# Optimization experiments

Hardware: AMD Instinct MI355X
Metric: run time of the kernel (lower is better)

Reference implementation:

```python
import jax, jax.numpy as jnp
import numpy as np

N_NODES = 50000
N_EDGES = 800000
F_IN = 64
F_OUT = 64
SELF_LOOP_W = 2.0  # GCNConv improved=True


def setup_inputs() -> dict:
    key = jax.random.key(0)
    k1, k2, k3 = jax.random.split(key, 3)
    x = jax.random.normal(k1, (N_NODES, F_IN), dtype=jnp.float32)
    edge_index = jax.random.randint(k2, (2, N_EDGES), 0, N_NODES, dtype=jnp.int64)
    W = jax.random.normal(k3, (F_IN, F_OUT), dtype=jnp.float32) / np.sqrt(F_IN)
    b = jnp.zeros((F_OUT,), dtype=jnp.float32)
    return {"x": x, "edge_index": edge_index, "W": W, "b": b}


def reference(x, edge_index, W, b):
    N = x.shape[0]
    E = edge_index.shape[1]
    src, dst = edge_index[0], edge_index[1]
    # add self loops with weight 2.0 (improved=True)
    loop = jnp.arange(N, dtype=src.dtype)
    src_f = jnp.concatenate([src, loop])
    dst_f = jnp.concatenate([dst, loop])
    w_edge = jnp.concatenate([jnp.ones((E,), x.dtype), jnp.full((N,), SELF_LOOP_W, x.dtype)])
    # symmetric normalization: deg over target nodes (PyG gcn_norm)
    deg = jax.ops.segment_sum(w_edge, dst_f, num_segments=N)
    dinv = jnp.where(deg > 0, deg ** -0.5, 0.0)
    norm = dinv[src_f] * w_edge * dinv[dst_f]  # [E+N]
    # dense transform, then gather-scale-scatter
    h = x @ W  # [N, F_OUT]
    agg = jax.ops.segment_sum(norm[:, None] * h[src_f], dst_f, num_segments=N)
    out = jax.nn.relu(agg + b)
    return jax.nn.log_softmax(out, axis=1)
```

## Files before the change

### kernel.cpp

```cpp
#include <hip/hip_runtime.h>
#include <hip/hip_fp16.h>

#define N_NODES 50000
#define N_EDGES 800000
#define F 64
#define NB ((N_NODES + 255) / 256)
#define NBUCK 98
#define BSHIFT 9
#define BCAP 12288
#define P1_BLOCKS ((N_EDGES + 1023) / 1024)
#define NPB 32


union H2U { __half2 h; unsigned u; };

__global__ __launch_bounds__(1024) void k_p1c(const int* __restrict__ src,
                                              const int* __restrict__ dst,
                                              int* __restrict__ bcur,
                                              int* __restrict__ staging,
                                              const float4* __restrict__ x4,
                                              uint2* __restrict__ xh8) {
    __shared__ int lcnt[NBUCK];
    __shared__ int lbase[NBUCK];
    int t = threadIdx.x;
    int g = blockIdx.x * 1024 + t;
    if (t < NBUCK) lcnt[t] = 0;
    if (g < N_NODES * (F / 4)) {
        float4 v = x4[g];
        H2U a, b;
        a.h = __float22half2_rn(make_float2(v.x, v.y));
        b.h = __float22half2_rn(make_float2(v.z, v.w));
        uint2 o; o.x = a.u; o.y = b.u;
        xh8[g] = o;
    }
    __syncthreads();
    int s = 0, d = 0, bk = 0, rank = 0;
    bool valid = (g < N_EDGES);
    if (valid) {
        s = src[g]; d = dst[g];
        bk = d >> BSHIFT;
        rank = atomicAdd(&lcnt[bk], 1);
    }
    __syncthreads();
    if (t < NBUCK && lcnt[t]) lbase[t] = atomicAdd(&bcur[t], lcnt[t]);
    __syncthreads();
    if (valid)
        staging[bk * BCAP + lbase[bk] + rank] = ((d & 511) << 16) | s;
}

__global__ __launch_bounds__(1024) void k_p23(const int* __restrict__ staging,
                                              const int* __restrict__ bcur,
                                              int* __restrict__ offsets,
                                              int* __restrict__ counts,
                                              float* __restrict__ dinv,
                                              int* __restrict__ pack) {
    __shared__ int ncnt[512];
    __shared__ int lcur[512];
    int t = threadIdx.x;
    int b = blockIdx.x;
    int nb0 = b << BSHIFT;
    if (t < 512) ncnt[t] = 0;
    __syncthreads();
    int beg = b * BCAP, end = beg + bcur[b];
    for (int i = beg + t; i < end; i += 1024)
        atomicAdd(&ncnt[staging[i] >> 16], 1);
    __syncthreads();
    int c = (t < 512) ? ncnt[t] : 0;
    for (int off = 1; off < 512; off <<= 1) {
        int u = (t < 512 && t >= off) ? ncnt[t - off] : 0;
        __syncthreads();
        if (t < 512) ncnt[t] += u;
        __syncthreads();
    }
    if (t < 512) {
        int goff = beg + (ncnt[t] - c);
        lcur[t] = goff;
        int node = nb0 + t;
        if (node < N_NODES) {
            offsets[node] = goff;
            counts[node]  = c;
            dinv[node]    = rsqrtf((float)c + 2.0f);
        }
    }
    __syncthreads();
    for (int i = beg + t; i < end; i += 1024) {
        int v = staging[i];
        int pos = atomicAdd(&lcur[v >> 16], 1);
        pack[pos] = v & 0xFFFF;
    }
}

__global__ __launch_bounds__(512) void k_agg(const float* __restrict__ x,
                                             const __half* __restrict__ xh,
                                             const float* __restrict__ dinv,
                                             const int* __restrict__ offsets,
                                             const int* __restrict__ counts,
                                             const int* __restrict__ pack,
                                             const float* __restrict__ W,
                                             const float* __restrict__ bias,
                                             float* __restrict__ out) {
    __shared__ unsigned sWu[F * F / 2];
    __shared__ float srow[NPB][F];
    int t = threadIdx.x;
    for (int i = t; i < F * F / 2; i += 512) {
        int p = i >> 6, c = i & 63;
        H2U u;
        u.h = __float22half2_rn(make_float2(W[(2 * p) * F + c], W[(2 * p + 1) * F + c]));
        sWu[i] = u.u;
    }
    __syncthreads();

    int wid = t >> 6, lane = t & 63;
    int qe = lane >> 4, qc = lane & 15;
    int nbase = blockIdx.x * NPB + wid * 4;
    const uint2* xh8 = reinterpret_cast<const uint2*>(xh);

    int4   off4 = *reinterpret_cast<const int4*>(offsets + nbase);
    int4   cnt4 = *reinterpret_cast<const int4*>(counts + nbase);
    float4 dv4  = *reinterpret_cast<const float4*>(dinv + nbase);
    int   begs[4] = { off4.x, off4.y, off4.z, off4.w };
    int   degs[4] = { cnt4.x, cnt4.y, cnt4.z, cnt4.w };
    float dns[4]  = { dv4.x, dv4.y, dv4.z, dv4.w };
#pragma unroll
    for (int i = 0; i < 4; ++i)
        if (nbase + i >= N_NODES) { degs[i] = 0; dns[i] = 0.f; begs[i] = 0; }

    int pls[4]; float nms[4];
#pragma unroll
    for (int i = 0; i < 4; ++i) {
        int s = 0; float nm = 0.f;
        if (lane < degs[i]) {
            s = pack[begs[i] + lane];
            nm = dns[i] * dinv[s];
        }
        pls[i] = s; nms[i] = nm;
    }

    float acc[4][4];
#pragma unroll
    for (int i = 0; i < 4; ++i)
#pragma unroll
        for (int j = 0; j < 4; ++j) acc[i][j] = 0.f;

    int lim = max(max(degs[0], degs[1]), max(degs[2], degs[3]));
    lim = min(lim, 64);
    for (int r = 0; r < lim; r += 8) {
        int e0 = r + qe, e1 = r + 4 + qe;
        uint2 v[4][2]; float m[4][2];
#pragma unroll
        for (int i = 0; i < 4; ++i) {
            int s0 = __shfl(pls[i], e0); m[i][0] = __shfl(nms[i], e0);
            int s1 = __shfl(pls[i], e1); m[i][1] = __shfl(nms[i], e1);
            v[i][0] = xh8[(size_t)s0 * 16 + qc];
            v[i][1] = xh8[(size_t)s1 * 16 + qc];
        }
#pragma unroll
        for (int i = 0; i < 4; ++i)
#pragma unroll
            for (int j = 0; j < 2; ++j) {
                H2U u0, u1;
                u0.u = v[i][j].x; u1.u = v[i][j].y;
                float2 f0 = __half22float2(u0.h);
                float2 f1 = __half22float2(u1.h);
                float mm = m[i][j];
                acc[i][0] = fmaf(mm, f0.x, acc[i][0]);
                acc[i][1] = fmaf(mm, f0.y, acc[i][1]);
                acc[i][2] = fmaf(mm, f1.x, acc[i][2]);
                acc[i][3] = fmaf(mm, f1.y, acc[i][3]);
            }
    }
#pragma unroll
    for (int i = 0; i < 4; ++i) {
        int dend = begs[i] + degs[i];
        for (int base = begs[i] + 64; base < dend; base += 8) {
            int e0 = base + qe, e1 = base + 4 + qe;
            int s0 = 0, s1 = 0; float m0 = 0.f, m1 = 0.f;
            if (e0 < dend) { s0 = pack[e0]; m0 = dns[i] * dinv[s0]; }
            if (e1 < dend) { s1 = pack[e1]; m1 = dns[i] * dinv[s1]; }
            uint2 r0 = xh8[(size_t)s0 * 16 + qc];
            uint2 r1 = xh8[(size_t)s1 * 16 + qc];
            H2U u0, u1; float2 f;
            u0.u = r0.x; u1.u = r0.y;
            f = __half22float2(u0.h); acc[i][0] = fmaf(m0, f.x, acc[i][0]); acc[i][1] = fmaf(m0, f.y, acc[i][1]);
            f = __half22float2(u1.h); acc[i][2] = fmaf(m0, f.x, acc[i][2]); acc[i][3] = fmaf(m0, f.y, acc[i][3]);
            u0.u = r1.x; u1.u = r1.y;
            f = __half22float2(u0.h); acc[i][0] = fmaf(m1, f.x, acc[i][0]); acc[i][1] = fmaf(m1, f.y, acc[i][1]);
            f = __half22float2(u1.h); acc[i][2] = fmaf(m1, f.x, acc[i][2]); acc[i][3] = fmaf(m1, f.y, acc[i][3]);
        }
    }

#pragma unroll
    for (int i = 0; i < 4; ++i)
#pragma unroll
        for (int j = 0; j < 4; ++j) {
            acc[i][j] += __shfl_xor(acc[i][j], 16);
            acc[i][j] += __shfl_xor(acc[i][j], 32);
        }

    if (qe == 0) {
#pragma unroll
        for (int i = 0; i < 4; ++i) {
            int n = nbase + i;
            if (n < N_NODES) {
                float c2 = 2.0f * dns[i] * dns[i];
                float4 xv = reinterpret_cast<const float4*>(x + (size_t)n * F)[qc];
                float4 w;
                w.x = fmaf(c2, xv.x, acc[i][0]);
                w.y = fmaf(c2, xv.y, acc[i][1]);
                w.z = fmaf(c2, xv.z, acc[i][2]);
                w.w = fmaf(c2, xv.w, acc[i][3]);
                *reinterpret_cast<float4*>(&srow[wid * 4 + i][qc * 4]) = w;
            }
        }
    }

    asm volatile("s_waitcnt lgkmcnt(0)" ::: "memory");

    float bl = bias[lane];
    float y0 = bl, y1 = bl, y2 = bl, y3 = bl;
#pragma unroll 4
    for (int j = 0; j < 16; ++j) {
        float4 r0 = *reinterpret_cast<const float4*>(&srow[wid * 4 + 0][j * 4]);
        float4 r1 = *reinterpret_cast<const float4*>(&srow[wid * 4 + 1][j * 4]);
        float4 r2 = *reinterpret_cast<const float4*>(&srow[wid * 4 + 2][j * 4]);
        float4 r3 = *reinterpret_cast<const float4*>(&srow[wid * 4 + 3][j * 4]);
        H2U ua, ub;
        ua.u = sWu[(2 * j) * F + lane];
        ub.u = sWu[(2 * j + 1) * F + lane];
        float2 wab = __half22float2(ua.h);
        float2 wcd = __half22float2(ub.h);
        y0 = fmaf(r0.x, wab.x, y0); y0 = fmaf(r0.y, wab.y, y0); y0 = fmaf(r0.z, wcd.x, y0); y0 = fmaf(r0.w, wcd.y, y0);
        y1 = fmaf(r1.x, wab.x, y1); y1 = fmaf(r1.y, wab.y, y1); y1 = fmaf(r1.z, wcd.x, y1); y1 = fmaf(r1.w, wcd.y, y1);
        y2 = fmaf(r2.x, wab.x, y2); y2 = fmaf(r2.y, wab.y, y2); y2 = fmaf(r2.z, wcd.x, y2); y2 = fmaf(r2.w, wcd.y, y2);
        y3 = fmaf(r3.x, wab.x, y3); y3 = fmaf(r3.y, wab.y, y3); y3 = fmaf(r3.z, wcd.x, y3); y3 = fmaf(r3.w, wcd.y, y3);
    }

    float ys[4] = { y0, y1, y2, y3 };
#pragma unroll
    for (int i = 0; i < 4; ++i) {
        float y = fmaxf(ys[i], 0.0f);
        float mx = y;
#pragma unroll
        for (int off = 32; off > 0; off >>= 1)
            mx = fmaxf(mx, __shfl_xor(mx, off));
        float ex = __expf(y - mx);
        float ss = ex;
#pragma unroll
        for (int off = 32; off > 0; off >>= 1)
            ss += __shfl_xor(ss, off);
        int n = nbase + i;
        if (n < N_NODES) out[n * F + lane] = y - mx - __logf(ss);
    }
}


__global__ void k_count_b(const int* __restrict__ dst, int* __restrict__ counts) {
    int e = blockIdx.x * blockDim.x + threadIdx.x;
    if (e < N_EDGES) atomicAdd(&counts[dst[e]], 1);
}
__global__ __launch_bounds__(256) void k_blocksum(const int* __restrict__ counts,
                                                  int* __restrict__ bs) {
    __shared__ int sh[256];
    int t = threadIdx.x;
    int g = blockIdx.x * 256 + t;
    int v = (g < N_NODES) ? counts[g] : 0;
    sh[t] = v;
    __syncthreads();
    for (int off = 128; off > 0; off >>= 1) {
        if (t < off) sh[t] += sh[t + off];
        __syncthreads();
    }
    if (t == 0) bs[blockIdx.x] = sh[0];
}
__global__ __launch_bounds__(256) void k_scanblocks(int* __restrict__ bs) {
    __shared__ int sh[256];
    int t = threadIdx.x;
    int v = (t < NB) ? bs[t] : 0;
    sh[t] = v;
    __syncthreads();
    for (int off = 1; off < 256; off <<= 1) {
        int u = (t >= off) ? sh[t - off] : 0;
        __syncthreads();
        sh[t] += u;
        __syncthreads();
    }
    if (t < NB) bs[t] = sh[t] - v;
}
__global__ __launch_bounds__(256) void k_offsets_b(int* __restrict__ counts,
                                                   const int* __restrict__ bs,
                                                   int* __restrict__ offsets,
                                                   float* __restrict__ dinv) {
    __shared__ int sh[256];
    int t = threadIdx.x;
    int g = blockIdx.x * 256 + t;
    int c = (g < N_NODES) ? counts[g] : 0;
    sh[t] = c;
    __syncthreads();
    for (int off = 1; off < 256; off <<= 1) {
        int u = (t >= off) ? sh[t - off] : 0;
        __syncthreads();
        sh[t] += u;
        __syncthreads();
    }
    int excl = sh[t] - c + bs[blockIdx.x];
    if (g < N_NODES) {
        offsets[g] = excl;
        counts[g]  = excl;
        dinv[g]    = rsqrtf((float)c + 2.0f);
    }
    if (g == 0) offsets[N_NODES] = N_EDGES;
}
__global__ void k_fill_b(const int* __restrict__ src, const int* __restrict__ dst,
                         int* __restrict__ cursor, int* __restrict__ sorted_src) {
    int e = blockIdx.x * blockDim.x + threadIdx.x;
    if (e < N_EDGES) {
        int pos = atomicAdd(&cursor[dst[e]], 1);
        sorted_src[pos] = src[e];
    }
}
__global__ __launch_bounds__(256) void k_agg_b(const float* __restrict__ x,
                                               const float* __restrict__ dinv,
                                               const int* __restrict__ offsets,
                                               const int* __restrict__ sorted_src,
                                               const float* __restrict__ W,
                                               const float* __restrict__ b,
                                               float* __restrict__ out) {
    __shared__ float sW[F * F];
    __shared__ float srow[4][F];
    int t = threadIdx.x;
    for (int i = t; i < F * F; i += 256) sW[i] = W[i];
    int wid = t >> 6, lane = t & 63;
    int n = blockIdx.x * 4 + wid;
    int qe = lane >> 4, qc = lane & 15;
    float dn = dinv[n];
    int beg = offsets[n], end = offsets[n + 1];
    float4 acc = make_float4(0.f, 0.f, 0.f, 0.f);
    for (int base = beg; base < end; base += 4) {
        int e = base + qe;
        int s = n; float nm = 0.f;
        if (e < end) { s = sorted_src[e]; nm = dn * dinv[s]; }
        float4 v = reinterpret_cast<const float4*>(x + (size_t)s * F)[qc];
        acc.x = fmaf(nm, v.x, acc.x); acc.y = fmaf(nm, v.y, acc.y);
        acc.z = fmaf(nm, v.z, acc.z); acc.w = fmaf(nm, v.w, acc.w);
    }
    acc.x += __shfl_xor(acc.x, 16); acc.y += __shfl_xor(acc.y, 16);
    acc.z += __shfl_xor(acc.z, 16); acc.w += __shfl_xor(acc.w, 16);
    acc.x += __shfl_xor(acc.x, 32); acc.y += __shfl_xor(acc.y, 32);
    acc.z += __shfl_xor(acc.z, 32); acc.w += __shfl_xor(acc.w, 32);
    float c2 = 2.0f * dn * dn;
    float4 xv = reinterpret_cast<const float4*>(x + (size_t)n * F)[qc];
    acc.x = fmaf(c2, xv.x, acc.x); acc.y = fmaf(c2, xv.y, acc.y);
    acc.z = fmaf(c2, xv.z, acc.z); acc.w = fmaf(c2, xv.w, acc.w);
    if (qe == 0) reinterpret_cast<float4*>(&srow[wid][0])[qc] = acc;
    __syncthreads();
    float y = b[lane];
#pragma unroll
    for (int k = 0; k < F; ++k) y = fmaf(srow[wid][k], sW[k * F + lane], y);
    y = fmaxf(y, 0.0f);
    float m = y;
#pragma unroll
    for (int off = 32; off > 0; off >>= 1) m = fmaxf(m, __shfl_xor(m, off));
    float ex = __expf(y - m);
    float ss = ex;
#pragma unroll
    for (int off = 32; off > 0; off >>= 1) ss += __shfl_xor(ss, off);
    out[n * F + lane] = y - m - __logf(ss);
}


__global__ void k_init_deg_f(float* __restrict__ deg) {
    int i = blockIdx.x * blockDim.x + threadIdx.x;
    if (i < N_NODES) deg[i] = 2.0f;
}
__global__ void k_count_f(const int* __restrict__ dst, float* __restrict__ deg) {
    int e = blockIdx.x * blockDim.x + threadIdx.x;
    if (e < N_EDGES) atomicAdd(&deg[dst[e]], 1.0f);
}
__global__ void k_dinv_f(float* __restrict__ deg) {
    int i = blockIdx.x * blockDim.x + threadIdx.x;
    if (i < N_NODES) deg[i] = rsqrtf(deg[i]);
}
__global__ void k_selfinit_f(const float* __restrict__ x, const float* __restrict__ dinv,
                             float* __restrict__ agg) {
    int t = blockIdx.x * blockDim.x + threadIdx.x;
    if (t >= N_NODES * (F / 4)) return;
    int n = t >> 4;
    float d = dinv[n];
    float c = 2.0f * d * d;
    float4 v = reinterpret_cast<const float4*>(x)[t];
    float4 o; o.x = c*v.x; o.y = c*v.y; o.z = c*v.z; o.w = c*v.w;
    reinterpret_cast<float4*>(agg)[t] = o;
}
__global__ __launch_bounds__(256) void k_scatter_f(const int* __restrict__ src,
                                                   const int* __restrict__ dst,
                                                   const float* __restrict__ x,
                                                   const float* __restrict__ dinv,
                                                   float* __restrict__ agg) {
    int wave = (blockIdx.x * blockDim.x + threadIdx.x) >> 6;
    int lane = threadIdx.x & 63;
    if (wave >= N_EDGES) return;
    int s = src[wave], d = dst[wave];
    atomicAdd(&agg[d * F + lane], dinv[s] * dinv[d] * x[s * F + lane]);
}
__global__ __launch_bounds__(256) void k_final_f(const float* __restrict__ W,
                                                 const float* __restrict__ b,
                                                 float* __restrict__ out) {
    __shared__ float sW[F * F];
    __shared__ float srow[4][F];
    int t = threadIdx.x;
    for (int i = t; i < F * F; i += 256) sW[i] = W[i];
    int wid = t >> 6, lane = t & 63;
    int n = blockIdx.x * 4 + wid;
    float rv = out[n * F + lane];
    srow[wid][lane] = rv;
    __syncthreads();
    float y = b[lane];
#pragma unroll
    for (int k = 0; k < F; ++k) y = fmaf(srow[wid][k], sW[k * F + lane], y);
    y = fmaxf(y, 0.0f);
    float m = y;
#pragma unroll
    for (int off = 32; off > 0; off >>= 1) m = fmaxf(m, __shfl_xor(m, off));
    float ex = __expf(y - m);
    float ss = ex;
#pragma unroll
    for (int off = 32; off > 0; off >>= 1) ss += __shfl_xor(ss, off);
    out[n * F + lane] = y - m - __logf(ss);
}


extern "C" void kernel_launch(void* const* d_in, const int* in_sizes, int n_in,
                              void* d_out, int out_size, void* d_ws, size_t ws_size,
                              hipStream_t stream) {
    const float* x    = (const float*)d_in[0];
    const int*   eidx = (const int*)d_in[1];
    const float* W    = (const float*)d_in[2];
    const float* b    = (const float*)d_in[3];
    const int* src = eidx;
    const int* dst = eidx + N_EDGES;
    float* out = (float*)d_out;

    const size_t NEED_A5 = 11818112;
    const size_t NEED_B  = 3801040;

    if (ws_size >= NEED_A5) {
        char* ws = (char*)d_ws;
        int*    offsets = (int*)(ws);
        int*    counts  = (int*)(ws + 200064);
        float*  dinv    = (float*)(ws + 400128);
        int*    bcur    = (int*)(ws + 600192);
        int*    pack    = (int*)(ws + 601216);
        __half* xh      = (__half*)(ws + 5418112);
        int*    staging = (int*)d_out;

        hipMemsetAsync(bcur, 0, NBUCK * sizeof(int), stream);
        k_p1c<<<P1_BLOCKS, 1024, 0, stream>>>(src, dst, bcur, staging,
                                              (const float4*)x, (uint2*)xh);
        k_p23<<<NBUCK, 1024, 0, stream>>>(staging, bcur, offsets, counts, dinv, pack);
        k_agg<<<(N_NODES + NPB - 1) / NPB, 512, 0, stream>>>(
            x, xh, dinv, offsets, counts, pack, W, b, out);
    } else if (ws_size >= NEED_B) {
        char* ws = (char*)d_ws;
        int*   counts     = (int*)(ws);
        int*   offsets    = (int*)(ws + 200000);
        float* dinv       = (float*)(ws + 400016);
        int*   bs         = (int*)(ws + 600016);
        int*   sorted_src = (int*)(ws + 601040);

        hipMemsetAsync(counts, 0, N_NODES * sizeof(int), stream);
        k_count_b<<<(N_EDGES + 255) / 256, 256, 0, stream>>>(dst, counts);
        k_blocksum<<<NB, 256, 0, stream>>>(counts, bs);
        k_scanblocks<<<1, 256, 0, stream>>>(bs);
        k_offsets_b<<<NB, 256, 0, stream>>>(counts, bs, offsets, dinv);
        k_fill_b<<<(N_EDGES + 255) / 256, 256, 0, stream>>>(src, dst, counts, sorted_src);
        k_agg_b<<<N_NODES / 4, 256, 0, stream>>>(x, dinv, offsets, sorted_src, W, b, out);
    } else {
        float* deg = (float*)d_ws;
        k_init_deg_f<<<(N_NODES + 255) / 256, 256, 0, stream>>>(deg);
        k_count_f<<<(N_EDGES + 255) / 256, 256, 0, stream>>>(dst, deg);
        k_dinv_f<<<(N_NODES + 255) / 256, 256, 0, stream>>>(deg);
        k_selfinit_f<<<(N_NODES * (F / 4) + 255) / 256, 256, 0, stream>>>(x, deg, out);
        k_scatter_f<<<(N_EDGES * 64 + 255) / 256, 256, 0, stream>>>(src, dst, x, deg, out);
        k_final_f<<<N_NODES / 4, 256, 0, stream>>>(W, b, out);
    }
}
```

Before: 89.97 us.

## Precompute half-precision edge norms in pack and simplify aggregation to lane-per-feature

The fused bucket-sort kernel is split in two. A new pass computes each edge's symmetric norm (dinv[src]*dinv[dst]) and packs it as fp16 into the upper bits of the pack entry next to the source index. Aggregation drops the shuffle-based 16-lane quad scheme and uses one lane per feature with a wave-uniform loop over edges, reading 2-byte fp16 features per lane and the self-loop term from the fp16 copy of x. The memset becomes a tiny init kernel. This removes per-edge dinv gathers in the hot loop, but adds a kernel launch and lowers precision for norms and the self term.

After: 108.6 us. +20.7%, slower.

```diff
diff --git a/kernel.cpp b/kernel.cpp
--- a/kernel.cpp
+++ b/kernel.cpp
@@ -14,6 +14,11 @@
 
 union H2U { __half2 h; unsigned u; };
 
+__global__ void k_init(int* __restrict__ bcur) {
+    int t = threadIdx.x;
+    if (t < NBUCK) bcur[t] = 0;
+}
+
 __global__ __launch_bounds__(1024) void k_p1c(const int* __restrict__ src,
                                               const int* __restrict__ dst,
                                               int* __restrict__ bcur,
@@ -48,14 +53,12 @@
         staging[bk * BCAP + lbase[bk] + rank] = ((d & 511) << 16) | s;
 }
 
-__global__ __launch_bounds__(1024) void k_p23(const int* __restrict__ staging,
-                                              const int* __restrict__ bcur,
-                                              int* __restrict__ offsets,
-                                              int* __restrict__ counts,
-                                              float* __restrict__ dinv,
-                                              int* __restrict__ pack) {
+__global__ __launch_bounds__(1024) void k_p2(const int* __restrict__ staging,
+                                             const int* __restrict__ bcur,
+                                             int* __restrict__ offsets,
+                                             int* __restrict__ counts,
+                                             float* __restrict__ dinv) {
     __shared__ int ncnt[512];
-    __shared__ int lcur[512];
     int t = threadIdx.x;
     int b = blockIdx.x;
     int nb0 = b << BSHIFT;
@@ -73,29 +76,48 @@
         __syncthreads();
     }
     if (t < 512) {
-        int goff = beg + (ncnt[t] - c);
-        lcur[t] = goff;
         int node = nb0 + t;
         if (node < N_NODES) {
-            offsets[node] = goff;
+            offsets[node] = beg + (ncnt[t] - c);
             counts[node]  = c;
             dinv[node]    = rsqrtf((float)c + 2.0f);
         }
     }
-    __syncthreads();
+}
+
+__global__ __launch_bounds__(1024) void k_p3(const int* __restrict__ staging,
+                                             const int* __restrict__ bcur,
+                                             const int* __restrict__ offsets,
+                                             const float* __restrict__ dinv,
+                                             unsigned* __restrict__ pack) {
+    __shared__ int lcur[512];
+    __shared__ float sdinv[512];
+    int t = threadIdx.x;
+    int b = blockIdx.x;
+    int nb0 = b << BSHIFT;
+    if (t < 512) {
+        int node = nb0 + t;
+        lcur[t]  = (node < N_NODES) ? offsets[node] : 0;
+        sdinv[t] = (node < N_NODES) ? dinv[node] : 0.f;
+    }
+    __syncthreads();
+    int beg = b * BCAP, end = beg + bcur[b];
     for (int i = beg + t; i < end; i += 1024) {
         int v = staging[i];
-        int pos = atomicAdd(&lcur[v >> 16], 1);
-        pack[pos] = v & 0xFFFF;
-    }
-}
-
-__global__ __launch_bounds__(512) void k_agg(const float* __restrict__ x,
-                                             const __half* __restrict__ xh,
+        int dl = v >> 16;
+        int s  = v & 0xFFFF;
+        int pos = atomicAdd(&lcur[dl], 1);
+        float nm = dinv[s] * sdinv[dl];
+        unsigned hv = __half_as_ushort(__float2half_rn(nm));
+        pack[pos] = (hv << 16) | (unsigned)s;
+    }
+}
+
+__global__ __launch_bounds__(512) void k_agg(const __half* __restrict__ xh,
                                              const float* __restrict__ dinv,
                                              const int* __restrict__ offsets,
                                              const int* __restrict__ counts,
-                                             const int* __restrict__ pack,
+                                             const unsigned* __restrict__ pack,
                                              const float* __restrict__ W,
                                              const float* __restrict__ bias,
                                              float* __restrict__ out) {
@@ -111,106 +133,44 @@
     __syncthreads();
 
     int wid = t >> 6, lane = t & 63;
-    int qe = lane >> 4, qc = lane & 15;
     int nbase = blockIdx.x * NPB + wid * 4;
-    const uint2* xh8 = reinterpret_cast<const uint2*>(xh);
-
-    int4   off4 = *reinterpret_cast<const int4*>(offsets + nbase);
-    int4   cnt4 = *reinterpret_cast<const int4*>(counts + nbase);
-    float4 dv4  = *reinterpret_cast<const float4*>(dinv + nbase);
-    int   begs[4] = { off4.x, off4.y, off4.z, off4.w };
-    int   degs[4] = { cnt4.x, cnt4.y, cnt4.z, cnt4.w };
-    float dns[4]  = { dv4.x, dv4.y, dv4.z, dv4.w };
-#pragma unroll
-    for (int i = 0; i < 4; ++i)
-        if (nbase + i >= N_NODES) { degs[i] = 0; dns[i] = 0.f; begs[i] = 0; }
-
-    int pls[4]; float nms[4];
+
 #pragma unroll
     for (int i = 0; i < 4; ++i) {
-        int s = 0; float nm = 0.f;
-        if (lane < degs[i]) {
-            s = pack[begs[i] + lane];
-            nm = dns[i] * dinv[s];
+        int n = nbase + i;
+        int beg = 0, deg = 0; float dn = 0.f;
+        if (n < N_NODES) {
+            beg = __builtin_amdgcn_readfirstlane(offsets[n]);
+            deg = __builtin_amdgcn_readfirstlane(counts[n]);
+            dn  = dinv[n];
         }
-        pls[i] = s; nms[i] = nm;
-    }
-
-    float acc[4][4];
-#pragma unroll
-    for (int i = 0; i < 4; ++i)
-#pragma unroll
-        for (int j = 0; j < 4; ++j) acc[i][j] = 0.f;
-
-    int lim = max(max(degs[0], degs[1]), max(degs[2], degs[3]));
-    lim = min(lim, 64);
-    for (int r = 0; r < lim; r += 8) {
-        int e0 = r + qe, e1 = r + 4 + qe;
-        uint2 v[4][2]; float m[4][2];
-#pragma unroll
-        for (int i = 0; i < 4; ++i) {
-            int s0 = __shfl(pls[i], e0); m[i][0] = __shfl(nms[i], e0);
-            int s1 = __shfl(pls[i], e1); m[i][1] = __shfl(nms[i], e1);
-            v[i][0] = xh8[(size_t)s0 * 16 + qc];
-            v[i][1] = xh8[(size_t)s1 * 16 + qc];
+
+        float a0 = 0.f, a1 = 0.f, a2 = 0.f, a3 = 0.f;
+        int e = 0;
+        for (; e + 4 <= deg; e += 4) {
+            unsigned p0 = pack[beg + e + 0];
+            unsigned p1 = pack[beg + e + 1];
+            unsigned p2 = pack[beg + e + 2];
+            unsigned p3 = pack[beg + e + 3];
+            float v0 = __half2float(xh[(size_t)(p0 & 0xFFFF) * F + lane]);
+            float v1 = __half2float(xh[(size_t)(p1 & 0xFFFF) * F + lane]);
+            float v2 = __half2float(xh[(size_t)(p2 & 0xFFFF) * F + lane]);
+            float v3 = __half2float(xh[(size_t)(p3 & 0xFFFF) * F + lane]);
+            a0 = fmaf(__half2float(__ushort_as_half((unsigned short)(p0 >> 16))), v0, a0);
+            a1 = fmaf(__half2float(__ushort_as_half((unsigned short)(p1 >> 16))), v1, a1);
+            a2 = fmaf(__half2float(__ushort_as_half((unsigned short)(p2 >> 16))), v2, a2);
+            a3 = fmaf(__half2float(__ushort_as_half((unsigned short)(p3 >> 16))), v3, a3);
         }
-#pragma unroll
-        for (int i = 0; i < 4; ++i)
-#pragma unroll
-            for (int j = 0; j < 2; ++j) {
-                H2U u0, u1;
-                u0.u = v[i][j].x; u1.u = v[i][j].y;
-                float2 f0 = __half22float2(u0.h);
-                float2 f1 = __half22float2(u1.h);
-                float mm = m[i][j];
-                acc[i][0] = fmaf(mm, f0.x, acc[i][0]);
-                acc[i][1] = fmaf(mm, f0.y, acc[i][1]);
-                acc[i][2] = fmaf(mm, f1.x, acc[i][2]);
-                acc[i][3] = fmaf(mm, f1.y, acc[i][3]);
-            }
-    }
-#pragma unroll
-    for (int i = 0; i < 4; ++i) {
-        int dend = begs[i] + degs[i];
-        for (int base = begs[i] + 64; base < dend; base += 8) {
-            int e0 = base + qe, e1 = base + 4 + qe;
-            int s0 = 0, s1 = 0; float m0 = 0.f, m1 = 0.f;
-            if (e0 < dend) { s0 = pack[e0]; m0 = dns[i] * dinv[s0]; }
-            if (e1 < dend) { s1 = pack[e1]; m1 = dns[i] * dinv[s1]; }
-            uint2 r0 = xh8[(size_t)s0 * 16 + qc];
-            uint2 r1 = xh8[(size_t)s1 * 16 + qc];
-            H2U u0, u1; float2 f;
-            u0.u = r0.x; u1.u = r0.y;
-            f = __half22float2(u0.h); acc[i][0] = fmaf(m0, f.x, acc[i][0]); acc[i][1] = fmaf(m0, f.y, acc[i][1]);
-            f = __half22float2(u1.h); acc[i][2] = fmaf(m0, f.x, acc[i][2]); acc[i][3] = fmaf(m0, f.y, acc[i][3]);
-            u0.u = r1.x; u1.u = r1.y;
-            f = __half22float2(u0.h); acc[i][0] = fmaf(m1, f.x, acc[i][0]); acc[i][1] = fmaf(m1, f.y, acc[i][1]);
-            f = __half22float2(u1.h); acc[i][2] = fmaf(m1, f.x, acc[i][2]); acc[i][3] = fmaf(m1, f.y, acc[i][3]);
+        for (; e < deg; ++e) {
+            unsigned p0 = pack[beg + e];
+            float v0 = __half2float(xh[(size_t)(p0 & 0xFFFF) * F + lane]);
+            a0 = fmaf(__half2float(__ushort_as_half((unsigned short)(p0 >> 16))), v0, a0);
         }
-    }
-
-#pragma unroll
-    for (int i = 0; i < 4; ++i)
-#pragma unroll
-        for (int j = 0; j < 4; ++j) {
-            acc[i][j] += __shfl_xor(acc[i][j], 16);
-            acc[i][j] += __shfl_xor(acc[i][j], 32);
-        }
-
-    if (qe == 0) {
-#pragma unroll
-        for (int i = 0; i < 4; ++i) {
-            int n = nbase + i;
-            if (n < N_NODES) {
-                float c2 = 2.0f * dns[i] * dns[i];
-                float4 xv = reinterpret_cast<const float4*>(x + (size_t)n * F)[qc];
-                float4 w;
-                w.x = fmaf(c2, xv.x, acc[i][0]);
-                w.y = fmaf(c2, xv.y, acc[i][1]);
-                w.z = fmaf(c2, xv.z, acc[i][2]);
-                w.w = fmaf(c2, xv.w, acc[i][3]);
-                *reinterpret_cast<float4*>(&srow[wid * 4 + i][qc * 4]) = w;
-            }
+        float acc = (a0 + a1) + (a2 + a3);
+        if (n < N_NODES) {
+            float sv = __half2float(xh[(size_t)n * F + lane]);
+            acc = fmaf(2.0f * dn * dn, sv, acc);
+            srow[wid * 4 + i][lane] = acc;
         }
     }
 
@@ -440,25 +400,26 @@
     const int* dst = eidx + N_EDGES;
     float* out = (float*)d_out;
 
-    const size_t NEED_A5 = 11818112;
+    const size_t NEED_A8 = 11818112;
     const size_t NEED_B  = 3801040;
 
-    if (ws_size >= NEED_A5) {
+    if (ws_size >= NEED_A8) {
         char* ws = (char*)d_ws;
-        int*    offsets = (int*)(ws);
-        int*    counts  = (int*)(ws + 200064);
-        float*  dinv    = (float*)(ws + 400128);
-        int*    bcur    = (int*)(ws + 600192);
-        int*    pack    = (int*)(ws + 601216);
-        __half* xh      = (__half*)(ws + 5418112);
-        int*    staging = (int*)d_out;
-
-        hipMemsetAsync(bcur, 0, NBUCK * sizeof(int), stream);
+        int*      offsets = (int*)(ws);
+        int*      counts  = (int*)(ws + 200064);
+        float*    dinv    = (float*)(ws + 400128);
+        int*      bcur    = (int*)(ws + 600192);
+        unsigned* pack    = (unsigned*)(ws + 601216);
+        __half*   xh      = (__half*)(ws + 5418112);
+        int*      staging = (int*)d_out;
+
+        k_init<<<1, 128, 0, stream>>>(bcur);
         k_p1c<<<P1_BLOCKS, 1024, 0, stream>>>(src, dst, bcur, staging,
                                               (const float4*)x, (uint2*)xh);
-        k_p23<<<NBUCK, 1024, 0, stream>>>(staging, bcur, offsets, counts, dinv, pack);
+        k_p2<<<NBUCK, 1024, 0, stream>>>(staging, bcur, offsets, counts, dinv);
+        k_p3<<<NBUCK, 1024, 0, stream>>>(staging, bcur, offsets, dinv, pack);
         k_agg<<<(N_NODES + NPB - 1) / NPB, 512, 0, stream>>>(
-            x, xh, dinv, offsets, counts, pack, W, b, out);
+            xh, dinv, offsets, counts, pack, W, b, out);
     } else if (ws_size >= NEED_B) {
         char* ws = (char*)d_ws;
         int*   counts     = (int*)(ws);
```
